# Performance work log

Hardware: AMD Instinct MI355X
Metric: run time of the kernel (lower is better)

Reference implementation:

```python
import jax, jax.numpy as jnp
import numpy as np

N = 50000      # nodes
E = 600000     # edges (before self-loops)
F_IN = 128     # num_node_features
HID = 64       # hidden_channels
HEADS = 4      # num_heads
ACT = 32       # action_dim
SENT = 768     # sentence embedding dim (fc1 input)


def setup_inputs() -> dict:
    key = jax.random.key(0)
    ks = jax.random.split(key, 32)
    rn = lambda k, s, sc=0.05: jax.random.normal(k, s, jnp.float32) * sc
    return {
        "x": jax.random.normal(ks[0], (N, F_IN), jnp.float32),
        "edge_index": jax.random.randint(ks[1], (2, E), 0, N, dtype=jnp.int32),
        "sentence_emb": jax.random.normal(ks[2], (1, SENT), jnp.float32),
        "active_node_idx": 123,
        "step": 3,
        # conv1: GATConv(F_IN -> HID, heads=HEADS, concat=True)
        "W1": rn(ks[3], (F_IN, HEADS * HID)),
        "att_src1": rn(ks[4], (HEADS, HID)),
        "att_dst1": rn(ks[5], (HEADS, HID)),
        "b1": jnp.zeros((HEADS * HID,), jnp.float32),
        # conv2: GATConv(HEADS*HID -> HID, heads=1, concat=False)
        "W2": rn(ks[6], (HEADS * HID, HID)),
        "att_src2": rn(ks[7], (1, HID)),
        "att_dst2": rn(ks[8], (1, HID)),
        "b2": jnp.zeros((HID,), jnp.float32),
        "fc0_w": rn(ks[9], (1, HID)), "fc0_b": jnp.zeros((HID,), jnp.float32),
        "fc1_w": rn(ks[10], (SENT, HID)), "fc1_b": jnp.zeros((HID,), jnp.float32),
        "fc2_w": rn(ks[11], (HID, HID)), "fc2_b": jnp.zeros((HID,), jnp.float32),
        "fc3_w": rn(ks[12], (2 * HID, HID)), "fc3_b": jnp.zeros((HID,), jnp.float32),
        "val_w": rn(ks[13], (HID, 1)), "val_b": jnp.zeros((1,), jnp.float32),
        "adv_w": rn(ks[14], (HID, ACT)), "adv_b": jnp.zeros((ACT,), jnp.float32),
        "ln_h_g": jnp.ones((HID,), jnp.float32), "ln_h_b": jnp.zeros((HID,), jnp.float32),
        "ln_f_g": jnp.ones((2 * HID,), jnp.float32), "ln_f_b": jnp.zeros((2 * HID,), jnp.float32),
        "ln_a_g": jnp.ones((HEADS * HID,), jnp.float32), "ln_a_b": jnp.zeros((HEADS * HID,), jnp.float32),
    }


def layernorm(x, g, b, eps=1e-5):
    mu = jnp.mean(x, axis=-1, keepdims=True)
    var = jnp.mean((x - mu) ** 2, axis=-1, keepdims=True)
    return (x - mu) / jnp.sqrt(var + eps) * g + b


def gat_layer(h_in, src, dst, W, a_src, a_dst, bias, concat):
    """PyG GATConv (eval mode): gather -> edge score -> segment softmax -> scatter-add."""
    n = h_in.shape[0]
    heads, ch = a_src.shape
    h = (h_in @ W).reshape(n, heads, ch)                      # [N,H,C]
    es = jnp.einsum('nhc,hc->nh', h, a_src)                   # alpha_src per node
    ed = jnp.einsum('nhc,hc->nh', h, a_dst)                   # alpha_dst per node
    e = jax.nn.leaky_relu(es[src] + ed[dst], 0.2)             # [Etot,H]
    m = jax.ops.segment_max(e, dst, num_segments=n)           # stable softmax per dst
    ex = jnp.exp(e - m[dst])
    denom = jax.ops.segment_sum(ex, dst, num_segments=n) + 1e-16
    alpha = ex / denom[dst]                                   # [Etot,H]
    out = jax.ops.segment_sum(h[src] * alpha[:, :, None], dst, num_segments=n)
    out = out.reshape(n, heads * ch) if concat else out.mean(axis=1)
    return out + bias, alpha


def reference(x, edge_index, sentence_emb, active_node_idx, step,
              W1, att_src1, att_dst1, b1, W2, att_src2, att_dst2, b2,
              fc0_w, fc0_b, fc1_w, fc1_b, fc2_w, fc2_b, fc3_w, fc3_b,
              val_w, val_b, adv_w, adv_b,
              ln_h_g, ln_h_b, ln_f_g, ln_f_b, ln_a_g, ln_a_b):
    n = x.shape[0]
    loops = jnp.arange(n, dtype=edge_index.dtype)             # PyG add_self_loops=True
    src = jnp.concatenate([edge_index[0], loops])
    dst = jnp.concatenate([edge_index[1], loops])

    # step embedding: fc0((step+1)*0.01) -> relu -> LN
    steps = jnp.full((1, 1), (step + 1) * 0.01, jnp.float32)
    steps = layernorm(jax.nn.relu(steps @ fc0_w + fc0_b), ln_h_g, ln_h_b)

    # sentence embedding path (F.normalize result is discarded in the original)
    sent = layernorm(jax.nn.relu(sentence_emb @ fc1_w + fc1_b), ln_h_g, ln_h_b)
    sent = sent + steps
    sent = layernorm(jax.nn.relu(sent @ fc2_w + fc2_b), ln_h_g, ln_h_b)

    # two GAT layers
    h1, _ = gat_layer(x, src, dst, W1, att_src1, att_dst1, b1, concat=True)
    h1 = layernorm(jax.nn.elu(h1), ln_a_g, ln_a_b)
    h2, alpha = gat_layer(h1, src, dst, W2, att_src2, att_dst2, b2, concat=False)
    h2 = layernorm(h2, ln_h_g, ln_h_b)

    # dueling head on active node
    anf = jnp.concatenate([h2[active_node_idx][None, :], sent], axis=1)   # [1, 2*HID]
    anf = layernorm(anf, ln_f_g, ln_f_b)
    anf = layernorm(jax.nn.relu(anf @ fc3_w + fc3_b), ln_h_g, ln_h_b)
    val = anf @ val_w + val_b
    adv = anf @ adv_w + adv_b
    logits = jnp.tanh(val + adv - adv.mean())
    return logits, h2, alpha
```

## Files before the change

kernel.cpp:

```cpp
#include <hip/hip_runtime.h>
#include <cstdint>
#include <cstddef>

#define DEV __device__ __forceinline__

static constexpr int NN  = 50000;
static constexpr int EE  = 600000;
static constexpr int ET  = 650000;
static constexpr int SCAN_CHUNK = 1024;
static constexpr int SCAN_NB = (NN + SCAN_CHUNK - 1) / SCAN_CHUNK;

typedef __attribute__((ext_vector_type(8))) short bf16x8;
typedef __attribute__((ext_vector_type(4))) float f32x4;
typedef __attribute__((ext_vector_type(4))) int   i32x4;

DEV float wsum(float v){
  #pragma unroll
  for (int o = 32; o > 0; o >>= 1) v += __shfl_xor(v, o, 64);
  return v;
}
DEV float wmaxr(float v){
  #pragma unroll
  for (int o = 32; o > 0; o >>= 1) v = fmaxf(v, __shfl_xor(v, o, 64));
  return v;
}
DEV float lrelu(float x){ return x > 0.f ? x : 0.2f * x; }
DEV float eluf(float x){ return x > 0.f ? x : expm1f(x); }
DEV float ln64(float v, const float* g, const float* b, int lane){
  float mu  = wsum(v) * (1.f/64.f);
  float d   = v - mu;
  float var = wsum(d*d) * (1.f/64.f);
  return d * rsqrtf(var + 1e-5f) * g[lane] + b[lane];
}
DEV unsigned int bf16u(float f){
  unsigned int u = __float_as_uint(f);
  return (u + 0x7fffu + ((u >> 16) & 1u)) >> 16;
}
DEV float bfl(unsigned int lo16){ return __uint_as_float(lo16 << 16); }

__global__ void degree_kernel(const int* __restrict__ ei, int* __restrict__ deg){
  int e = blockIdx.x * blockDim.x + threadIdx.x;
  if (e >= ET) return;
  int dst = (e < EE) ? ei[EE + e] : (e - EE);
  atomicAdd(&deg[dst], 1);
}

__global__ __launch_bounds__(256) void scan_part(const int* __restrict__ deg,
                                                 int* __restrict__ off,
                                                 int* __restrict__ bsum, int n){
  __shared__ int wtot[4];
  int tid = threadIdx.x, lane = tid & 63, w = tid >> 6;
  int i0 = blockIdx.x * SCAN_CHUNK + tid * 4;
  int v[4], s = 0;
  #pragma unroll
  for (int p = 0; p < 4; p++){ int i = i0 + p; v[p] = (i < n) ? deg[i] : 0; s += v[p]; }
  int sc = s;
  #pragma unroll
  for (int d = 1; d < 64; d <<= 1){ int t = __shfl_up(sc, d, 64); if (lane >= d) sc += t; }
  if (lane == 63) wtot[w] = sc;
  __syncthreads();
  int woff = 0;
  #pragma unroll
  for (int k = 0; k < 4; k++) if (k < w) woff += wtot[k];
  int excl = woff + sc - s;
  #pragma unroll
  for (int p = 0; p < 4; p++){
    int i = i0 + p;
    if (i < n) off[i] = excl;
    excl += v[p];
  }
  if (tid == 0) bsum[blockIdx.x] = wtot[0] + wtot[1] + wtot[2] + wtot[3];
}

__global__ __launch_bounds__(64) void scan_top(int* __restrict__ bsum, int nb){
  int lane = threadIdx.x;
  int v = (lane < nb) ? bsum[lane] : 0;
  int sc = v;
  #pragma unroll
  for (int d = 1; d < 64; d <<= 1){ int t = __shfl_up(sc, d, 64); if (lane >= d) sc += t; }
  if (lane < nb) bsum[lane] = sc - v;
  if (lane == 63) bsum[nb] = sc;
}

__global__ __launch_bounds__(256) void scan_add(int* __restrict__ off,
                                                int* __restrict__ cur,
                                                const int* __restrict__ bsum, int n, int nb){
  int i0 = blockIdx.x * SCAN_CHUNK + threadIdx.x * 4;
  int add = bsum[blockIdx.x];
  #pragma unroll
  for (int p = 0; p < 4; p++){
    int j = i0 + p;
    if (j < n){ int t = off[j] + add; off[j] = t; cur[j] = t; }
  }
  if (blockIdx.x == 0 && threadIdx.x == 0) off[n] = bsum[nb];
}

__global__ void fill_csr(const int* __restrict__ ei, int* __restrict__ cur,
                         int* __restrict__ csr_src, int* __restrict__ csr_eid){
  int e = blockIdx.x * blockDim.x + threadIdx.x;
  if (e >= ET) return;
  int src, dst;
  if (e < EE){ src = ei[e]; dst = ei[EE + e]; } else { src = dst = e - EE; }
  int pos = atomicAdd(&cur[dst], 1);
  csr_src[pos] = src;
  csr_eid[pos] = e;
}

__global__ __launch_bounds__(256) void pack_w(const float* __restrict__ W,
                                              short* __restrict__ Wp, int K, int N){
  int tid = blockIdx.x * blockDim.x + threadIdx.x;
  int ksteps = K >> 5;
  int total = (N >> 4) * ksteps * 64;
  if (tid >= total) return;
  int lane = tid & 63;
  int ks   = (tid >> 6) % ksteps;
  int mb   = (tid >> 6) / ksteps;
  int col  = mb * 16 + (lane & 15);
  int krow = ks * 32 + (lane >> 4) * 8;
  short v[8];
  #pragma unroll
  for (int j = 0; j < 8; j++) v[j] = (short)bf16u(W[(size_t)(krow + j) * N + col]);
  #pragma unroll
  for (int j = 0; j < 8; j++) Wp[(size_t)tid * 8 + j] = v[j];
}

template<int KSTEPS, int MBLKS, int NH, bool INF32>
__global__ __launch_bounds__(256) void mfma_gemm_att(const short* __restrict__ Wp,
                                                     const float* __restrict__ Xf,
                                                     const unsigned short* __restrict__ Xh,
                                                     unsigned short* __restrict__ Cb,
                                                     const float* __restrict__ asrc,
                                                     const float* __restrict__ adst,
                                                     float* __restrict__ es,
                                                     float* __restrict__ ed, int M){
  constexpr int K = KSTEPS * 32, N = MBLKS * 16;
  int lane  = threadIdx.x & 63;
  int wv    = threadIdx.x >> 6;
  int quad  = lane >> 4;
  int node  = blockIdx.x * 64 + wv * 16 + (lane & 15);
  bool nv   = node < M;
  int nodec = nv ? node : M - 1;

  f32x4 acc[MBLKS];
  #pragma unroll
  for (int m = 0; m < MBLKS; m++) acc[m] = (f32x4){0.f, 0.f, 0.f, 0.f};

  #pragma unroll
  for (int ks = 0; ks < KSTEPS; ks++){
    int k0 = ks * 32 + quad * 8;
    bf16x8 bfrag;
    if (INF32){
      float4 u = *(const float4*)(Xf + (size_t)nodec * K + k0);
      float4 v = *(const float4*)(Xf + (size_t)nodec * K + k0 + 4);
      i32x4 bi;
      bi.x = (int)(bf16u(u.x) | (bf16u(u.y) << 16));
      bi.y = (int)(bf16u(u.z) | (bf16u(u.w) << 16));
      bi.z = (int)(bf16u(v.x) | (bf16u(v.y) << 16));
      bi.w = (int)(bf16u(v.z) | (bf16u(v.w) << 16));
      bfrag = __builtin_bit_cast(bf16x8, bi);
    } else {
      bfrag = *(const bf16x8*)(Xh + (size_t)nodec * K + k0);
    }
    #pragma unroll
    for (int mb = 0; mb < MBLKS; mb++){
      bf16x8 afrag = *(const bf16x8*)(Wp + ((size_t)(mb * KSTEPS + ks) * 64 + lane) * 8);
      acc[mb] = __builtin_amdgcn_mfma_f32_16x16x32_bf16(afrag, bfrag, acc[mb], 0, 0, 0);
    }
  }

  if (nv){
    unsigned short* crow = Cb + (size_t)node * N;
    #pragma unroll
    for (int mb = 0; mb < MBLKS; mb++){
      uint2 p;
      p.x = bf16u(acc[mb][0]) | (bf16u(acc[mb][1]) << 16);
      p.y = bf16u(acc[mb][2]) | (bf16u(acc[mb][3]) << 16);
      *(uint2*)(crow + mb * 16 + quad * 4) = p;
    }
  }

  float ps[NH], pd[NH];
  #pragma unroll
  for (int h = 0; h < NH; h++){ ps[h] = 0.f; pd[h] = 0.f; }
  #pragma unroll
  for (int mb = 0; mb < MBLKS; mb++){
    int h = (NH == 1) ? 0 : (mb >> 2);
    #pragma unroll
    for (int r = 0; r < 4; r++){
      int c = mb * 16 + quad * 4 + r;
      ps[h] = fmaf(acc[mb][r], asrc[c], ps[h]);
      pd[h] = fmaf(acc[mb][r], adst[c], pd[h]);
    }
  }
  #pragma unroll
  for (int h = 0; h < NH; h++){
    ps[h] += __shfl_xor(ps[h], 16, 64); ps[h] += __shfl_xor(ps[h], 32, 64);
    pd[h] += __shfl_xor(pd[h], 16, 64); pd[h] += __shfl_xor(pd[h], 32, 64);
  }
  if (quad == 0 && nv){
    if (NH == 4){
      *(float4*)(es + (size_t)node * 4) = make_float4(ps[0], ps[1], ps[2], ps[3]);
      *(float4*)(ed + (size_t)node * 4) = make_float4(pd[0], pd[1], pd[2], pd[3]);
    } else {
      es[node] = ps[0];
      ed[node] = pd[0];
    }
  }
}

__global__ __launch_bounds__(256) void agg1_kernel(const int* __restrict__ off,
                                                   const int* __restrict__ csr_src,
                                                   const unsigned short* __restrict__ H1b,
                                                   const float* __restrict__ es,
                                                   const float* __restrict__ ed,
                                                   const float* __restrict__ b1,
                                                   const float* __restrict__ lng,
                                                   const float* __restrict__ lnb,
                                                   unsigned short* __restrict__ h1b, int n){
  __shared__ float wsh4[4][64][4];
  __shared__ int   ssh[4][64];
  int wv   = threadIdx.x >> 6;
  int wid  = (blockIdx.x * blockDim.x + threadIdx.x) >> 6;
  int lane = threadIdx.x & 63;
  if (wid >= n) return;
  int s0  = off[wid];
  int deg = off[wid + 1] - s0;
  const float4 edv = *(const float4*)(ed + (size_t)wid * 4);

  float v0, v1, v2, v3;

  if (deg <= 64){
    bool vld = lane < deg;
    int srcl = vld ? csr_src[s0 + lane] : 0;
    float4 e4 = vld ? *(const float4*)(es + (size_t)srcl * 4)
                    : make_float4(-1e30f, -1e30f, -1e30f, -1e30f);
    float e0 = vld ? lrelu(e4.x + edv.x) : -1e30f;
    float e1 = vld ? lrelu(e4.y + edv.y) : -1e30f;
    float e2 = vld ? lrelu(e4.z + edv.z) : -1e30f;
    float e3 = vld ? lrelu(e4.w + edv.w) : -1e30f;
    float m0 = wmaxr(e0), m1 = wmaxr(e1), m2 = wmaxr(e2), m3 = wmaxr(e3);
    float w0 = vld ? __expf(e0 - m0) : 0.f;
    float w1 = vld ? __expf(e1 - m1) : 0.f;
    float w2 = vld ? __expf(e2 - m2) : 0.f;
    float w3 = vld ? __expf(e3 - m3) : 0.f;
    w0 /= (wsum(w0) + 1e-16f);
    w1 /= (wsum(w1) + 1e-16f);
    w2 /= (wsum(w2) + 1e-16f);
    w3 /= (wsum(w3) + 1e-16f);
    ssh[wv][lane] = srcl;
    *(float4*)&wsh4[wv][lane][0] = make_float4(w0, w1, w2, w3);
    __builtin_amdgcn_wave_barrier();

    int h = lane >> 4;
    float ax = 0.f, ay = 0.f, az = 0.f, aw = 0.f;
    int t = 0;
    for (; t + 4 <= deg; t += 4){
      int a0 = ssh[wv][t],     a1 = ssh[wv][t + 1];
      int a2 = ssh[wv][t + 2], a3 = ssh[wv][t + 3];
      float q0 = wsh4[wv][t][h],     q1 = wsh4[wv][t + 1][h];
      float q2 = wsh4[wv][t + 2][h], q3 = wsh4[wv][t + 3][h];
      uint2 g0 = *(const uint2*)(H1b + (size_t)a0 * 256 + lane * 4);
      uint2 g1 = *(const uint2*)(H1b + (size_t)a1 * 256 + lane * 4);
      uint2 g2 = *(const uint2*)(H1b + (size_t)a2 * 256 + lane * 4);
      uint2 g3 = *(const uint2*)(H1b + (size_t)a3 * 256 + lane * 4);
      ax = fmaf(__uint_as_float(g0.x << 16),        q0, ax);
      ay = fmaf(__uint_as_float(g0.x & 0xffff0000u), q0, ay);
      az = fmaf(__uint_as_float(g0.y << 16),        q0, az);
      aw = fmaf(__uint_as_float(g0.y & 0xffff0000u), q0, aw);
      ax = fmaf(__uint_as_float(g1.x << 16),        q1, ax);
      ay = fmaf(__uint_as_float(g1.x & 0xffff0000u), q1, ay);
      az = fmaf(__uint_as_float(g1.y << 16),        q1, az);
      aw = fmaf(__uint_as_float(g1.y & 0xffff0000u), q1, aw);
      ax = fmaf(__uint_as_float(g2.x << 16),        q2, ax);
      ay = fmaf(__uint_as_float(g2.x & 0xffff0000u), q2, ay);
      az = fmaf(__uint_as_float(g2.y << 16),        q2, az);
      aw = fmaf(__uint_as_float(g2.y & 0xffff0000u), q2, aw);
      ax = fmaf(__uint_as_float(g3.x << 16),        q3, ax);
      ay = fmaf(__uint_as_float(g3.x & 0xffff0000u), q3, ay);
      az = fmaf(__uint_as_float(g3.y << 16),        q3, az);
      aw = fmaf(__uint_as_float(g3.y & 0xffff0000u), q3, aw);
    }
    for (; t < deg; t++){
      int a0 = ssh[wv][t];
      float q0 = wsh4[wv][t][h];
      uint2 g0 = *(const uint2*)(H1b + (size_t)a0 * 256 + lane * 4);
      ax = fmaf(__uint_as_float(g0.x << 16),        q0, ax);
      ay = fmaf(__uint_as_float(g0.x & 0xffff0000u), q0, ay);
      az = fmaf(__uint_as_float(g0.y << 16),        q0, az);
      aw = fmaf(__uint_as_float(g0.y & 0xffff0000u), q0, aw);
    }
    float4 bb = *(const float4*)(b1 + lane * 4);
    v0 = eluf(ax + bb.x); v1 = eluf(ay + bb.y);
    v2 = eluf(az + bb.z); v3 = eluf(aw + bb.w);
    float mu = wsum(v0 + v1 + v2 + v3) * (1.f/256.f);
    float q  = (v0-mu)*(v0-mu) + (v1-mu)*(v1-mu) + (v2-mu)*(v2-mu) + (v3-mu)*(v3-mu);
    float rstd = rsqrtf(wsum(q) * (1.f/256.f) + 1e-5f);
    float4 g4 = *(const float4*)(lng + lane * 4);
    float4 bo = *(const float4*)(lnb + lane * 4);
    uint2 p;
    p.x = bf16u((v0-mu)*rstd*g4.x + bo.x) | (bf16u((v1-mu)*rstd*g4.y + bo.y) << 16);
    p.y = bf16u((v2-mu)*rstd*g4.z + bo.z) | (bf16u((v3-mu)*rstd*g4.w + bo.w) << 16);
    *(uint2*)(h1b + (size_t)wid * 256 + lane * 4) = p;
    return;
  }

  float m0 = -1e30f, m1 = -1e30f, m2 = -1e30f, m3 = -1e30f;
  for (int j = lane; j < deg; j += 64){
    int src = csr_src[s0 + j];
    float4 e4 = *(const float4*)(es + (size_t)src * 4);
    m0 = fmaxf(m0, lrelu(e4.x + edv.x));
    m1 = fmaxf(m1, lrelu(e4.y + edv.y));
    m2 = fmaxf(m2, lrelu(e4.z + edv.z));
    m3 = fmaxf(m3, lrelu(e4.w + edv.w));
  }
  m0 = wmaxr(m0); m1 = wmaxr(m1); m2 = wmaxr(m2); m3 = wmaxr(m3);
  float acc0 = 0.f, acc1 = 0.f, acc2 = 0.f, acc3 = 0.f;
  float den0 = 0.f, den1 = 0.f, den2 = 0.f, den3 = 0.f;
  for (int j = 0; j < deg; j++){
    int src = csr_src[s0 + j];
    float4 e4 = *(const float4*)(es + (size_t)src * 4);
    float x0 = __expf(lrelu(e4.x + edv.x) - m0);
    float x1 = __expf(lrelu(e4.y + edv.y) - m1);
    float x2 = __expf(lrelu(e4.z + edv.z) - m2);
    float x3 = __expf(lrelu(e4.w + edv.w) - m3);
    den0 += x0; den1 += x1; den2 += x2; den3 += x3;
    const unsigned short* hp = H1b + (size_t)src * 256;
    acc0 = fmaf(bfl(hp[lane]),       x0, acc0);
    acc1 = fmaf(bfl(hp[64 + lane]),  x1, acc1);
    acc2 = fmaf(bfl(hp[128 + lane]), x2, acc2);
    acc3 = fmaf(bfl(hp[192 + lane]), x3, acc3);
  }
  v0 = eluf(acc0 / (den0 + 1e-16f) + b1[lane]);
  v1 = eluf(acc1 / (den1 + 1e-16f) + b1[64 + lane]);
  v2 = eluf(acc2 / (den2 + 1e-16f) + b1[128 + lane]);
  v3 = eluf(acc3 / (den3 + 1e-16f) + b1[192 + lane]);
  float mu = wsum(v0 + v1 + v2 + v3) * (1.f/256.f);
  float q  = (v0-mu)*(v0-mu) + (v1-mu)*(v1-mu) + (v2-mu)*(v2-mu) + (v3-mu)*(v3-mu);
  float rstd = rsqrtf(wsum(q) * (1.f/256.f) + 1e-5f);
  unsigned short* o = h1b + (size_t)wid * 256;
  o[lane]       = (unsigned short)bf16u((v0-mu)*rstd*lng[lane]       + lnb[lane]);
  o[64 + lane]  = (unsigned short)bf16u((v1-mu)*rstd*lng[64 + lane]  + lnb[64 + lane]);
  o[128 + lane] = (unsigned short)bf16u((v2-mu)*rstd*lng[128 + lane] + lnb[128 + lane]);
  o[192 + lane] = (unsigned short)bf16u((v3-mu)*rstd*lng[192 + lane] + lnb[192 + lane]);
}

__global__ __launch_bounds__(256) void agg2_kernel(const int* __restrict__ off,
                                                   const int* __restrict__ csr_src,
                                                   const int* __restrict__ csr_eid,
                                                   const unsigned short* __restrict__ H2b,
                                                   const float* __restrict__ es,
                                                   const float* __restrict__ ed,
                                                   const float* __restrict__ b2,
                                                   const float* __restrict__ lng,
                                                   const float* __restrict__ lnb,
                                                   float* __restrict__ h2out,
                                                   float* __restrict__ alpha_out, int n){
  int wid  = (blockIdx.x * blockDim.x + threadIdx.x) >> 6;
  int lane = threadIdx.x & 63;
  if (wid >= n) return;
  int s0  = off[wid];
  int deg = off[wid + 1] - s0;
  float edv = ed[wid];
  float acc = 0.f;

  if (deg <= 64){
    bool vld = lane < deg;
    int srcl = vld ? csr_src[s0 + lane] : 0;
    float el = vld ? lrelu(es[srcl] + edv) : -1e30f;
    float m  = wmaxr(el);
    float w  = vld ? __expf(el - m) : 0.f;
    float den = wsum(w) + 1e-16f;
    float wl = w / den;
    if (vld) alpha_out[csr_eid[s0 + lane]] = wl;
    int t = 0;
    for (; t + 4 <= deg; t += 4){
      int a0 = __shfl(srcl, t, 64),   a1 = __shfl(srcl, t+1, 64);
      int a2 = __shfl(srcl, t+2, 64), a3 = __shfl(srcl, t+3, 64);
      float q0 = __shfl(wl, t, 64),   q1 = __shfl(wl, t+1, 64);
      float q2 = __shfl(wl, t+2, 64), q3 = __shfl(wl, t+3, 64);
      float h0 = bfl(H2b[(size_t)a0 * 64 + lane]);
      float h1v = bfl(H2b[(size_t)a1 * 64 + lane]);
      float h2v = bfl(H2b[(size_t)a2 * 64 + lane]);
      float h3 = bfl(H2b[(size_t)a3 * 64 + lane]);
      acc = fmaf(h0, q0, acc); acc = fmaf(h1v, q1, acc);
      acc = fmaf(h2v, q2, acc); acc = fmaf(h3, q3, acc);
    }
    for (; t < deg; t++){
      int a0 = __shfl(srcl, t, 64);
      float q0 = __shfl(wl, t, 64);
      acc = fmaf(bfl(H2b[(size_t)a0 * 64 + lane]), q0, acc);
    }
  } else {
    float m = -1e30f;
    for (int j = lane; j < deg; j += 64){
      int src = csr_src[s0 + j];
      m = fmaxf(m, lrelu(es[src] + edv));
    }
    m = wmaxr(m);
    float den = 0.f;
    for (int j = lane; j < deg; j += 64){
      int src = csr_src[s0 + j];
      den += __expf(lrelu(es[src] + edv) - m);
    }
    den = wsum(den) + 1e-16f;
    for (int j = 0; j < deg; j++){
      int src = csr_src[s0 + j];
      float a = __expf(lrelu(es[src] + edv) - m) / den;
      if (lane == 0) alpha_out[csr_eid[s0 + j]] = a;
      acc = fmaf(bfl(H2b[(size_t)src * 64 + lane]), a, acc);
    }
  }
  float v  = acc + b2[lane];
  float mu = wsum(v) * (1.f/64.f);
  float d  = v - mu;
  float rstd = rsqrtf(wsum(d*d) * (1.f/64.f) + 1e-5f);
  h2out[(size_t)wid * 64 + lane] = d * rstd * lng[lane] + lnb[lane];
}

__global__ __launch_bounds__(64) void head_kernel(const float* __restrict__ semb,
                                                  const int* __restrict__ active,
                                                  const int* __restrict__ step,
                                                  const float* __restrict__ fc0w, const float* __restrict__ fc0b,
                                                  const float* __restrict__ fc1w, const float* __restrict__ fc1b,
                                                  const float* __restrict__ fc2w, const float* __restrict__ fc2b,
                                                  const float* __restrict__ fc3w, const float* __restrict__ fc3b,
                                                  const float* __restrict__ valw, const float* __restrict__ valb,
                                                  const float* __restrict__ advw, const float* __restrict__ advb,
                                                  const float* __restrict__ lnhg, const float* __restrict__ lnhb,
                                                  const float* __restrict__ lnfg, const float* __restrict__ lnfb,
                                                  const float* __restrict__ h2,
                                                  float* __restrict__ out){
  int t = threadIdx.x;
  __shared__ float sh[128];

  float sval = (float)(step[0] + 1) * 0.01f;
  float stepsv = ln64(fmaxf(fmaf(sval, fc0w[t], fc0b[t]), 0.f), lnhg, lnhb, t);

  float acc = fc1b[t];
  #pragma unroll 8
  for (int k = 0; k < 768; k++) acc = fmaf(semb[k], fc1w[k * 64 + t], acc);
  float sentv = ln64(fmaxf(acc, 0.f), lnhg, lnhb, t) + stepsv;
  sh[t] = sentv;
  __syncthreads();
  float acc2 = fc2b[t];
  #pragma unroll 8
  for (int k = 0; k < 64; k++) acc2 = fmaf(sh[k], fc2w[k * 64 + t], acc2);
  __syncthreads();
  float sent2 = ln64(fmaxf(acc2, 0.f), lnhg, lnhb, t);

  float a0 = h2[(size_t)active[0] * 64 + t];
  float a1 = sent2;
  float mu = wsum(a0 + a1) * (1.f/128.f);
  float q  = (a0-mu)*(a0-mu) + (a1-mu)*(a1-mu);
  float rstd = rsqrtf(wsum(q) * (1.f/128.f) + 1e-5f);
  float n0 = (a0-mu)*rstd*lnfg[t]      + lnfb[t];
  float n1 = (a1-mu)*rstd*lnfg[64 + t] + lnfb[64 + t];
  sh[t] = n0; sh[64 + t] = n1;
  __syncthreads();

  float acc3 = fc3b[t];
  #pragma unroll 8
  for (int k = 0; k < 128; k++) acc3 = fmaf(sh[k], fc3w[k * 64 + t], acc3);
  float a2v = ln64(fmaxf(acc3, 0.f), lnhg, lnhb, t);
  __syncthreads();
  sh[t] = a2v;
  __syncthreads();

  float val = wsum(a2v * valw[t]) + valb[0];
  float advv = 0.f;
  if (t < 32){
    advv = advb[t];
    #pragma unroll 8
    for (int k = 0; k < 64; k++) advv = fmaf(sh[k], advw[k * 32 + t], advv);
  }
  float am = wsum(t < 32 ? advv : 0.f) * (1.f/32.f);
  if (t < 32) out[t] = tanhf(val + advv - am);
}

extern "C" void kernel_launch(void* const* d_in, const int* in_sizes, int n_in,
                              void* d_out, int out_size, void* d_ws, size_t ws_size,
                              hipStream_t stream) {
  const float* x     = (const float*)d_in[0];
  const int*   ei    = (const int*)  d_in[1];
  const float* semb  = (const float*)d_in[2];
  const int*   act   = (const int*)  d_in[3];
  const int*   step  = (const int*)  d_in[4];
  const float* W1    = (const float*)d_in[5];
  const float* as1   = (const float*)d_in[6];
  const float* ad1   = (const float*)d_in[7];
  const float* b1    = (const float*)d_in[8];
  const float* W2    = (const float*)d_in[9];
  const float* as2   = (const float*)d_in[10];
  const float* ad2   = (const float*)d_in[11];
  const float* b2    = (const float*)d_in[12];
  const float* fc0w  = (const float*)d_in[13];
  const float* fc0b  = (const float*)d_in[14];
  const float* fc1w  = (const float*)d_in[15];
  const float* fc1b  = (const float*)d_in[16];
  const float* fc2w  = (const float*)d_in[17];
  const float* fc2b  = (const float*)d_in[18];
  const float* fc3w  = (const float*)d_in[19];
  const float* fc3b  = (const float*)d_in[20];
  const float* valw  = (const float*)d_in[21];
  const float* valb  = (const float*)d_in[22];
  const float* advw  = (const float*)d_in[23];
  const float* advb  = (const float*)d_in[24];
  const float* lnhg  = (const float*)d_in[25];
  const float* lnhb  = (const float*)d_in[26];
  const float* lnfg  = (const float*)d_in[27];
  const float* lnfb  = (const float*)d_in[28];
  const float* lnag  = (const float*)d_in[29];
  const float* lnab  = (const float*)d_in[30];

  char* ws = (char*)d_ws;
  size_t o = 0;
  auto alloc = [&](size_t bytes) -> void* {
    o = (o + 255) & ~(size_t)255;
    void* p = ws + o;
    o += bytes;
    return p;
  };
  int*   deg     = (int*)  alloc((size_t)(NN + 1) * 4);
  int*   off     = (int*)  alloc((size_t)(NN + 1) * 4);
  int*   cur     = (int*)  alloc((size_t)NN * 4);
  int*   bsum    = (int*)  alloc((size_t)(SCAN_NB + 1) * 4);
  int*   csr_src = (int*)  alloc((size_t)ET * 4);
  int*   csr_eid = (int*)  alloc((size_t)ET * 4);
  short* Wp1     = (short*)alloc((size_t)16 * 4 * 64 * 8 * 2);
  short* Wp2     = (short*)alloc((size_t)4 * 8 * 64 * 8 * 2);
  unsigned short* H1b = (unsigned short*)alloc((size_t)NN * 256 * 2);
  unsigned short* h1b = (unsigned short*)alloc((size_t)NN * 256 * 2);
  float* es1     = (float*)alloc((size_t)NN * 16);
  float* ed1     = (float*)alloc((size_t)NN * 16);
  unsigned short* H2b = H1b;
  float* es2 = es1;
  float* ed2 = ed1;

  float* logits    = (float*)d_out;
  float* h2out     = (float*)d_out + 32;
  float* alpha_out = (float*)d_out + 32 + (size_t)NN * 64;

  hipMemsetAsync(deg, 0, (size_t)NN * 4, stream);
  degree_kernel<<<(ET + 255) / 256, 256, 0, stream>>>(ei, deg);
  scan_part<<<SCAN_NB, 256, 0, stream>>>(deg, off, bsum, NN);
  scan_top <<<1, 64, 0, stream>>>(bsum, SCAN_NB);
  scan_add <<<SCAN_NB, 256, 0, stream>>>(off, cur, bsum, NN, SCAN_NB);
  fill_csr<<<(ET + 255) / 256, 256, 0, stream>>>(ei, cur, csr_src, csr_eid);

  pack_w<<<16, 256, 0, stream>>>(W1, Wp1, 128, 256);
  pack_w<<<8, 256, 0, stream>>>(W2, Wp2, 256, 64);

  mfma_gemm_att<4, 16, 4, true><<<(NN + 63) / 64, 256, 0, stream>>>(
      Wp1, x, nullptr, H1b, as1, ad1, es1, ed1, NN);
  agg1_kernel<<<NN / 4, 256, 0, stream>>>(off, csr_src, H1b, es1, ed1, b1, lnag, lnab, h1b, NN);

  mfma_gemm_att<8, 4, 1, false><<<(NN + 63) / 64, 256, 0, stream>>>(
      Wp2, nullptr, h1b, H2b, as2, ad2, es2, ed2, NN);
  agg2_kernel<<<NN / 4, 256, 0, stream>>>(off, csr_src, csr_eid, H2b, es2, ed2, b2,
                                          lnhg, lnhb, h2out, alpha_out, NN);

  head_kernel<<<1, 64, 0, stream>>>(semb, act, step,
                                    fc0w, fc0b, fc1w, fc1b, fc2w, fc2b, fc3w, fc3b,
                                    valw, valb, advw, advb,
                                    lnhg, lnhb, lnfg, lnfb,
                                    h2out, logits);
}
```

Before: 393.5 us.

## Fuse CSR build into cooperative kernel, fuse head into agg2, retune aggregation loops

Replaces the memset, degree, three scan kernels, CSR fill and two weight-pack kernels with a single cooperative kernel that uses grid-wide syncs between phases, cutting launch overhead. The dueling head is folded into the second aggregation kernel and runs on the wave that owns the active node. The first aggregation now stores attention weights transposed and unrolls the gather by 8 with vector LDS loads. The second aggregation has each wave handle feature pairs per half-wave. In exchange, grid.sync costs and a 256-block cooperative grid limit parallelism for the atomic phases, and the head adds serial work inside one wave of agg2.

```diff
diff --git a/kernel.cpp b/kernel.cpp
--- a/kernel.cpp
+++ b/kernel.cpp
@@ -1,6 +1,9 @@
 #include <hip/hip_runtime.h>
+#include <hip/hip_cooperative_groups.h>
 #include <cstdint>
 #include <cstddef>
+
+namespace cg = cooperative_groups;
 
 #define DEV __device__ __forceinline__
 
@@ -38,90 +41,101 @@
 }
 DEV float bfl(unsigned int lo16){ return __uint_as_float(lo16 << 16); }
 
-__global__ void degree_kernel(const int* __restrict__ ei, int* __restrict__ deg){
-  int e = blockIdx.x * blockDim.x + threadIdx.x;
-  if (e >= ET) return;
-  int dst = (e < EE) ? ei[EE + e] : (e - EE);
-  atomicAdd(&deg[dst], 1);
-}
-
-__global__ __launch_bounds__(256) void scan_part(const int* __restrict__ deg,
-                                                 int* __restrict__ off,
-                                                 int* __restrict__ bsum, int n){
+__global__ __launch_bounds__(256) void prep_kernel(const int* __restrict__ ei,
+                                                   const float* __restrict__ W1,
+                                                   const float* __restrict__ W2,
+                                                   int* __restrict__ deg,
+                                                   int* __restrict__ off,
+                                                   int* __restrict__ cur,
+                                                   int* __restrict__ bsum,
+                                                   int* __restrict__ csr_src,
+                                                   int* __restrict__ csr_eid,
+                                                   short* __restrict__ Wp1,
+                                                   short* __restrict__ Wp2){
+  cg::grid_group grid = cg::this_grid();
+  const int tid = blockIdx.x * 256 + threadIdx.x;
   __shared__ int wtot[4];
-  int tid = threadIdx.x, lane = tid & 63, w = tid >> 6;
-  int i0 = blockIdx.x * SCAN_CHUNK + tid * 4;
-  int v[4], s = 0;
-  #pragma unroll
-  for (int p = 0; p < 4; p++){ int i = i0 + p; v[p] = (i < n) ? deg[i] : 0; s += v[p]; }
-  int sc = s;
-  #pragma unroll
-  for (int d = 1; d < 64; d <<= 1){ int t = __shfl_up(sc, d, 64); if (lane >= d) sc += t; }
-  if (lane == 63) wtot[w] = sc;
-  __syncthreads();
-  int woff = 0;
-  #pragma unroll
-  for (int k = 0; k < 4; k++) if (k < w) woff += wtot[k];
-  int excl = woff + sc - s;
-  #pragma unroll
-  for (int p = 0; p < 4; p++){
-    int i = i0 + p;
-    if (i < n) off[i] = excl;
-    excl += v[p];
-  }
-  if (tid == 0) bsum[blockIdx.x] = wtot[0] + wtot[1] + wtot[2] + wtot[3];
-}
-
-__global__ __launch_bounds__(64) void scan_top(int* __restrict__ bsum, int nb){
-  int lane = threadIdx.x;
-  int v = (lane < nb) ? bsum[lane] : 0;
-  int sc = v;
-  #pragma unroll
-  for (int d = 1; d < 64; d <<= 1){ int t = __shfl_up(sc, d, 64); if (lane >= d) sc += t; }
-  if (lane < nb) bsum[lane] = sc - v;
-  if (lane == 63) bsum[nb] = sc;
-}
-
-__global__ __launch_bounds__(256) void scan_add(int* __restrict__ off,
-                                                int* __restrict__ cur,
-                                                const int* __restrict__ bsum, int n, int nb){
-  int i0 = blockIdx.x * SCAN_CHUNK + threadIdx.x * 4;
-  int add = bsum[blockIdx.x];
-  #pragma unroll
-  for (int p = 0; p < 4; p++){
-    int j = i0 + p;
-    if (j < n){ int t = off[j] + add; off[j] = t; cur[j] = t; }
-  }
-  if (blockIdx.x == 0 && threadIdx.x == 0) off[n] = bsum[nb];
-}
-
-__global__ void fill_csr(const int* __restrict__ ei, int* __restrict__ cur,
-                         int* __restrict__ csr_src, int* __restrict__ csr_eid){
-  int e = blockIdx.x * blockDim.x + threadIdx.x;
-  if (e >= ET) return;
-  int src, dst;
-  if (e < EE){ src = ei[e]; dst = ei[EE + e]; } else { src = dst = e - EE; }
-  int pos = atomicAdd(&cur[dst], 1);
-  csr_src[pos] = src;
-  csr_eid[pos] = e;
-}
-
-__global__ __launch_bounds__(256) void pack_w(const float* __restrict__ W,
-                                              short* __restrict__ Wp, int K, int N){
-  int tid = blockIdx.x * blockDim.x + threadIdx.x;
-  int ksteps = K >> 5;
-  int total = (N >> 4) * ksteps * 64;
-  if (tid >= total) return;
-  int lane = tid & 63;
-  int ks   = (tid >> 6) % ksteps;
-  int mb   = (tid >> 6) / ksteps;
-  int col  = mb * 16 + (lane & 15);
-  int krow = ks * 32 + (lane >> 4) * 8;
-  short v[8];
-  #pragma unroll
-  for (int j = 0; j < 8; j++) v[j] = (short)bf16u(W[(size_t)(krow + j) * N + col]);
-  #pragma unroll
-  for (int j = 0; j < 8; j++) Wp[(size_t)tid * 8 + j] = v[j];
+
+  for (int i = tid; i <= NN; i += 65536) deg[i] = 0;
+  if (tid < 4096){
+    int lane = tid & 63, ks = (tid >> 6) & 3, mb = tid >> 8;
+    int col  = mb * 16 + (lane & 15);
+    int krow = ks * 32 + (lane >> 4) * 8;
+    #pragma unroll
+    for (int j = 0; j < 8; j++)
+      Wp1[(size_t)tid * 8 + j] = (short)bf16u(W1[(size_t)(krow + j) * 256 + col]);
+  } else if (tid < 4096 + 2048){
+    int t2 = tid - 4096;
+    int lane = t2 & 63, ks = (t2 >> 6) & 7, mb = t2 >> 9;
+    int col  = mb * 16 + (lane & 15);
+    int krow = ks * 32 + (lane >> 4) * 8;
+    #pragma unroll
+    for (int j = 0; j < 8; j++)
+      Wp2[(size_t)t2 * 8 + j] = (short)bf16u(W2[(size_t)(krow + j) * 64 + col]);
+  }
+  grid.sync();
+
+  for (int e = tid; e < ET; e += 65536){
+    int dst = (e < EE) ? ei[EE + e] : (e - EE);
+    atomicAdd(&deg[dst], 1);
+  }
+  grid.sync();
+
+  if (blockIdx.x < SCAN_NB){
+    int t = threadIdx.x, lane = t & 63, w = t >> 6;
+    int i0 = blockIdx.x * SCAN_CHUNK + t * 4;
+    int v[4], s = 0;
+    #pragma unroll
+    for (int p = 0; p < 4; p++){ int i = i0 + p; v[p] = (i < NN) ? deg[i] : 0; s += v[p]; }
+    int sc = s;
+    #pragma unroll
+    for (int d = 1; d < 64; d <<= 1){ int u = __shfl_up(sc, d, 64); if (lane >= d) sc += u; }
+    if (lane == 63) wtot[w] = sc;
+    __syncthreads();
+    int woff = 0;
+    #pragma unroll
+    for (int k = 0; k < 4; k++) if (k < w) woff += wtot[k];
+    int excl = woff + sc - s;
+    #pragma unroll
+    for (int p = 0; p < 4; p++){
+      int i = i0 + p;
+      if (i < NN) off[i] = excl;
+      excl += v[p];
+    }
+    if (t == 0) bsum[blockIdx.x] = wtot[0] + wtot[1] + wtot[2] + wtot[3];
+  }
+  grid.sync();
+
+  if (blockIdx.x == 0 && threadIdx.x < 64){
+    int lane = threadIdx.x;
+    int v = (lane < SCAN_NB) ? bsum[lane] : 0;
+    int sc = v;
+    #pragma unroll
+    for (int d = 1; d < 64; d <<= 1){ int u = __shfl_up(sc, d, 64); if (lane >= d) sc += u; }
+    if (lane < SCAN_NB) bsum[lane] = sc - v;
+    if (lane == 63) bsum[SCAN_NB] = sc;
+  }
+  grid.sync();
+
+  if (blockIdx.x < SCAN_NB){
+    int i0 = blockIdx.x * SCAN_CHUNK + threadIdx.x * 4;
+    int add = bsum[blockIdx.x];
+    #pragma unroll
+    for (int p = 0; p < 4; p++){
+      int j = i0 + p;
+      if (j < NN){ int u = off[j] + add; off[j] = u; cur[j] = u; }
+    }
+    if (blockIdx.x == 0 && threadIdx.x == 0) off[NN] = bsum[SCAN_NB];
+  }
+  grid.sync();
+
+  for (int e = tid; e < ET; e += 65536){
+    int src, dst;
+    if (e < EE){ src = ei[e]; dst = ei[EE + e]; } else { src = dst = e - EE; }
+    int pos = atomicAdd(&cur[dst], 1);
+    csr_src[pos] = src;
+    csr_eid[pos] = e;
+  }
 }
 
 template<int KSTEPS, int MBLKS, int NH, bool INF32>
@@ -208,6 +222,13 @@
   }
 }
 
+DEV void acc4u(uint2 g, float q, float& ax, float& ay, float& az, float& aw){
+  ax = fmaf(__uint_as_float(g.x << 16),         q, ax);
+  ay = fmaf(__uint_as_float(g.x & 0xffff0000u), q, ay);
+  az = fmaf(__uint_as_float(g.y << 16),         q, az);
+  aw = fmaf(__uint_as_float(g.y & 0xffff0000u), q, aw);
+}
+
 __global__ __launch_bounds__(256) void agg1_kernel(const int* __restrict__ off,
                                                    const int* __restrict__ csr_src,
                                                    const unsigned short* __restrict__ H1b,
@@ -217,7 +238,7 @@
                                                    const float* __restrict__ lng,
                                                    const float* __restrict__ lnb,
                                                    unsigned short* __restrict__ h1b, int n){
-  __shared__ float wsh4[4][64][4];
+  __shared__ float wshT[4][4][68];
   __shared__ int   ssh[4][64];
   int wv   = threadIdx.x >> 6;
   int wid  = (blockIdx.x * blockDim.x + threadIdx.x) >> 6;
@@ -248,59 +269,55 @@
     w2 /= (wsum(w2) + 1e-16f);
     w3 /= (wsum(w3) + 1e-16f);
     ssh[wv][lane] = srcl;
-    *(float4*)&wsh4[wv][lane][0] = make_float4(w0, w1, w2, w3);
+    wshT[wv][0][lane] = w0; wshT[wv][1][lane] = w1;
+    wshT[wv][2][lane] = w2; wshT[wv][3][lane] = w3;
     __builtin_amdgcn_wave_barrier();
 
     int h = lane >> 4;
+    const float* wrow = &wshT[wv][h][0];
+    int lane4 = lane * 4;
     float ax = 0.f, ay = 0.f, az = 0.f, aw = 0.f;
     int t = 0;
-    for (; t + 4 <= deg; t += 4){
-      int a0 = ssh[wv][t],     a1 = ssh[wv][t + 1];
-      int a2 = ssh[wv][t + 2], a3 = ssh[wv][t + 3];
-      float q0 = wsh4[wv][t][h],     q1 = wsh4[wv][t + 1][h];
-      float q2 = wsh4[wv][t + 2][h], q3 = wsh4[wv][t + 3][h];
-      uint2 g0 = *(const uint2*)(H1b + (size_t)a0 * 256 + lane * 4);
-      uint2 g1 = *(const uint2*)(H1b + (size_t)a1 * 256 + lane * 4);
-      uint2 g2 = *(const uint2*)(H1b + (size_t)a2 * 256 + lane * 4);
-      uint2 g3 = *(const uint2*)(H1b + (size_t)a3 * 256 + lane * 4);
-      ax = fmaf(__uint_as_float(g0.x << 16),        q0, ax);
-      ay = fmaf(__uint_as_float(g0.x & 0xffff0000u), q0, ay);
-      az = fmaf(__uint_as_float(g0.y << 16),        q0, az);
-      aw = fmaf(__uint_as_float(g0.y & 0xffff0000u), q0, aw);
-      ax = fmaf(__uint_as_float(g1.x << 16),        q1, ax);
-      ay = fmaf(__uint_as_float(g1.x & 0xffff0000u), q1, ay);
-      az = fmaf(__uint_as_float(g1.y << 16),        q1, az);
-      aw = fmaf(__uint_as_float(g1.y & 0xffff0000u), q1, aw);
-      ax = fmaf(__uint_as_float(g2.x << 16),        q2, ax);
-      ay = fmaf(__uint_as_float(g2.x & 0xffff0000u), q2, ay);
-      az = fmaf(__uint_as_float(g2.y << 16),        q2, az);
-      aw = fmaf(__uint_as_float(g2.y & 0xffff0000u), q2, aw);
-      ax = fmaf(__uint_as_float(g3.x << 16),        q3, ax);
-      ay = fmaf(__uint_as_float(g3.x & 0xffff0000u), q3, ay);
-      az = fmaf(__uint_as_float(g3.y << 16),        q3, az);
-      aw = fmaf(__uint_as_float(g3.y & 0xffff0000u), q3, aw);
+    for (; t + 8 <= deg; t += 8){
+      i32x4 sA = *(const i32x4*)&ssh[wv][t];
+      i32x4 sB = *(const i32x4*)&ssh[wv][t + 4];
+      f32x4 qA = *(const f32x4*)&wrow[t];
+      f32x4 qB = *(const f32x4*)&wrow[t + 4];
+      uint2 g0 = *(const uint2*)(H1b + (size_t)sA.x * 256 + lane4);
+      uint2 g1 = *(const uint2*)(H1b + (size_t)sA.y * 256 + lane4);
+      uint2 g2 = *(const uint2*)(H1b + (size_t)sA.z * 256 + lane4);
+      uint2 g3 = *(const uint2*)(H1b + (size_t)sA.w * 256 + lane4);
+      uint2 g4 = *(const uint2*)(H1b + (size_t)sB.x * 256 + lane4);
+      uint2 g5 = *(const uint2*)(H1b + (size_t)sB.y * 256 + lane4);
+      uint2 g6 = *(const uint2*)(H1b + (size_t)sB.z * 256 + lane4);
+      uint2 g7 = *(const uint2*)(H1b + (size_t)sB.w * 256 + lane4);
+      acc4u(g0, qA.x, ax, ay, az, aw);
+      acc4u(g1, qA.y, ax, ay, az, aw);
+      acc4u(g2, qA.z, ax, ay, az, aw);
+      acc4u(g3, qA.w, ax, ay, az, aw);
+      acc4u(g4, qB.x, ax, ay, az, aw);
+      acc4u(g5, qB.y, ax, ay, az, aw);
+      acc4u(g6, qB.z, ax, ay, az, aw);
+      acc4u(g7, qB.w, ax, ay, az, aw);
     }
     for (; t < deg; t++){
       int a0 = ssh[wv][t];
-      float q0 = wsh4[wv][t][h];
-      uint2 g0 = *(const uint2*)(H1b + (size_t)a0 * 256 + lane * 4);
-      ax = fmaf(__uint_as_float(g0.x << 16),        q0, ax);
-      ay = fmaf(__uint_as_float(g0.x & 0xffff0000u), q0, ay);
-      az = fmaf(__uint_as_float(g0.y << 16),        q0, az);
-      aw = fmaf(__uint_as_float(g0.y & 0xffff0000u), q0, aw);
-    }
-    float4 bb = *(const float4*)(b1 + lane * 4);
+      float q0 = wrow[t];
+      uint2 g0 = *(const uint2*)(H1b + (size_t)a0 * 256 + lane4);
+      acc4u(g0, q0, ax, ay, az, aw);
+    }
+    float4 bb = *(const float4*)(b1 + lane4);
     v0 = eluf(ax + bb.x); v1 = eluf(ay + bb.y);
     v2 = eluf(az + bb.z); v3 = eluf(aw + bb.w);
     float mu = wsum(v0 + v1 + v2 + v3) * (1.f/256.f);
     float q  = (v0-mu)*(v0-mu) + (v1-mu)*(v1-mu) + (v2-mu)*(v2-mu) + (v3-mu)*(v3-mu);
     float rstd = rsqrtf(wsum(q) * (1.f/256.f) + 1e-5f);
-    float4 g4 = *(const float4*)(lng + lane * 4);
-    float4 bo = *(const float4*)(lnb + lane * 4);
+    float4 g4v = *(const float4*)(lng + lane4);
+    float4 bo  = *(const float4*)(lnb + lane4);
     uint2 p;
-    p.x = bf16u((v0-mu)*rstd*g4.x + bo.x) | (bf16u((v1-mu)*rstd*g4.y + bo.y) << 16);
-    p.y = bf16u((v2-mu)*rstd*g4.z + bo.z) | (bf16u((v3-mu)*rstd*g4.w + bo.w) << 16);
-    *(uint2*)(h1b + (size_t)wid * 256 + lane * 4) = p;
+    p.x = bf16u((v0-mu)*rstd*g4v.x + bo.x) | (bf16u((v1-mu)*rstd*g4v.y + bo.y) << 16);
+    p.y = bf16u((v2-mu)*rstd*g4v.z + bo.z) | (bf16u((v3-mu)*rstd*g4v.w + bo.w) << 16);
+    *(uint2*)(h1b + (size_t)wid * 256 + lane4) = p;
     return;
   }
 
@@ -344,24 +361,42 @@
   o[192 + lane] = (unsigned short)bf16u((v3-mu)*rstd*lng[192 + lane] + lnb[192 + lane]);
 }
 
-__global__ __launch_bounds__(256) void agg2_kernel(const int* __restrict__ off,
-                                                   const int* __restrict__ csr_src,
-                                                   const int* __restrict__ csr_eid,
-                                                   const unsigned short* __restrict__ H2b,
-                                                   const float* __restrict__ es,
-                                                   const float* __restrict__ ed,
-                                                   const float* __restrict__ b2,
-                                                   const float* __restrict__ lng,
-                                                   const float* __restrict__ lnb,
-                                                   float* __restrict__ h2out,
-                                                   float* __restrict__ alpha_out, int n){
+__global__ __launch_bounds__(256) void agg2_head(const int* __restrict__ off,
+                                                 const int* __restrict__ csr_src,
+                                                 const int* __restrict__ csr_eid,
+                                                 const unsigned short* __restrict__ H2b,
+                                                 const float* __restrict__ es,
+                                                 const float* __restrict__ ed,
+                                                 const float* __restrict__ b2,
+                                                 const float* __restrict__ lng,
+                                                 const float* __restrict__ lnb,
+                                                 const float* __restrict__ semb,
+                                                 const int* __restrict__ active,
+                                                 const int* __restrict__ stepp,
+                                                 const float* __restrict__ fc0w, const float* __restrict__ fc0b,
+                                                 const float* __restrict__ fc1w, const float* __restrict__ fc1b,
+                                                 const float* __restrict__ fc2w, const float* __restrict__ fc2b,
+                                                 const float* __restrict__ fc3w, const float* __restrict__ fc3b,
+                                                 const float* __restrict__ valw, const float* __restrict__ valb,
+                                                 const float* __restrict__ advw, const float* __restrict__ advb,
+                                                 const float* __restrict__ lnhg, const float* __restrict__ lnhb,
+                                                 const float* __restrict__ lnfg, const float* __restrict__ lnfb,
+                                                 float* __restrict__ h2out,
+                                                 float* __restrict__ alpha_out,
+                                                 float* __restrict__ logits, int n){
+  __shared__ float wsa[4][64];
+  __shared__ int   ssa[4][64];
+  __shared__ float shh[192];
+  int wv   = threadIdx.x >> 6;
   int wid  = (blockIdx.x * blockDim.x + threadIdx.x) >> 6;
   int lane = threadIdx.x & 63;
   if (wid >= n) return;
   int s0  = off[wid];
   int deg = off[wid + 1] - s0;
   float edv = ed[wid];
-  float acc = 0.f;
+  int sub = lane & 31, half = lane >> 5;
+  const unsigned short* base = H2b + sub * 2;
+  float va, vb;
 
   if (deg <= 64){
     bool vld = lane < deg;
@@ -372,109 +407,120 @@
     float den = wsum(w) + 1e-16f;
     float wl = w / den;
     if (vld) alpha_out[csr_eid[s0 + lane]] = wl;
-    int t = 0;
-    for (; t + 4 <= deg; t += 4){
-      int a0 = __shfl(srcl, t, 64),   a1 = __shfl(srcl, t+1, 64);
-      int a2 = __shfl(srcl, t+2, 64), a3 = __shfl(srcl, t+3, 64);
-      float q0 = __shfl(wl, t, 64),   q1 = __shfl(wl, t+1, 64);
-      float q2 = __shfl(wl, t+2, 64), q3 = __shfl(wl, t+3, 64);
-      float h0 = bfl(H2b[(size_t)a0 * 64 + lane]);
-      float h1v = bfl(H2b[(size_t)a1 * 64 + lane]);
-      float h2v = bfl(H2b[(size_t)a2 * 64 + lane]);
-      float h3 = bfl(H2b[(size_t)a3 * 64 + lane]);
-      acc = fmaf(h0, q0, acc); acc = fmaf(h1v, q1, acc);
-      acc = fmaf(h2v, q2, acc); acc = fmaf(h3, q3, acc);
-    }
-    for (; t < deg; t++){
-      int a0 = __shfl(srcl, t, 64);
-      float q0 = __shfl(wl, t, 64);
-      acc = fmaf(bfl(H2b[(size_t)a0 * 64 + lane]), q0, acc);
-    }
+    ssa[wv][lane] = srcl;
+    wsa[wv][lane] = vld ? wl : 0.f;
+    __builtin_amdgcn_wave_barrier();
+
+    float a0 = 0.f, a1 = 0.f;
+    int nsteps = (deg + 1) >> 1;
+    int j = 0;
+    for (; j + 4 <= nsteps; j += 4){
+      int e0 = 2 * j + half;
+      int sA = ssa[wv][e0],     sB = ssa[wv][e0 + 2];
+      int sC = ssa[wv][e0 + 4], sD = ssa[wv][e0 + 6];
+      float wA = wsa[wv][e0],     wB = wsa[wv][e0 + 2];
+      float wC = wsa[wv][e0 + 4], wD = wsa[wv][e0 + 6];
+      unsigned int gA = *(const unsigned int*)(base + (size_t)sA * 64);
+      unsigned int gB = *(const unsigned int*)(base + (size_t)sB * 64);
+      unsigned int gC = *(const unsigned int*)(base + (size_t)sC * 64);
+      unsigned int gD = *(const unsigned int*)(base + (size_t)sD * 64);
+      a0 = fmaf(__uint_as_float(gA << 16),         wA, a0);
+      a1 = fmaf(__uint_as_float(gA & 0xffff0000u), wA, a1);
+      a0 = fmaf(__uint_as_float(gB << 16),         wB, a0);
+      a1 = fmaf(__uint_as_float(gB & 0xffff0000u), wB, a1);
+      a0 = fmaf(__uint_as_float(gC << 16),         wC, a0);
+      a1 = fmaf(__uint_as_float(gC & 0xffff0000u), wC, a1);
+      a0 = fmaf(__uint_as_float(gD << 16),         wD, a0);
+      a1 = fmaf(__uint_as_float(gD & 0xffff0000u), wD, a1);
+    }
+    for (; j < nsteps; j++){
+      int e = 2 * j + half;
+      int sA = ssa[wv][e];
+      float wA = wsa[wv][e];
+      unsigned int g = *(const unsigned int*)(base + (size_t)sA * 64);
+      a0 = fmaf(__uint_as_float(g << 16),         wA, a0);
+      a1 = fmaf(__uint_as_float(g & 0xffff0000u), wA, a1);
+    }
+    a0 += __shfl_xor(a0, 32, 64);
+    a1 += __shfl_xor(a1, 32, 64);
+    va = a0 + b2[2 * sub];
+    vb = a1 + b2[2 * sub + 1];
   } else {
     float m = -1e30f;
-    for (int j = lane; j < deg; j += 64){
-      int src = csr_src[s0 + j];
-      m = fmaxf(m, lrelu(es[src] + edv));
-    }
+    for (int j2 = lane; j2 < deg; j2 += 64)
+      m = fmaxf(m, lrelu(es[csr_src[s0 + j2]] + edv));
     m = wmaxr(m);
     float den = 0.f;
-    for (int j = lane; j < deg; j += 64){
-      int src = csr_src[s0 + j];
-      den += __expf(lrelu(es[src] + edv) - m);
-    }
+    for (int j2 = lane; j2 < deg; j2 += 64)
+      den += __expf(lrelu(es[csr_src[s0 + j2]] + edv) - m);
     den = wsum(den) + 1e-16f;
-    for (int j = 0; j < deg; j++){
-      int src = csr_src[s0 + j];
-      float a = __expf(lrelu(es[src] + edv) - m) / den;
-      if (lane == 0) alpha_out[csr_eid[s0 + j]] = a;
-      acc = fmaf(bfl(H2b[(size_t)src * 64 + lane]), a, acc);
-    }
-  }
-  float v  = acc + b2[lane];
-  float mu = wsum(v) * (1.f/64.f);
-  float d  = v - mu;
-  float rstd = rsqrtf(wsum(d*d) * (1.f/64.f) + 1e-5f);
-  h2out[(size_t)wid * 64 + lane] = d * rstd * lng[lane] + lnb[lane];
-}
-
-__global__ __launch_bounds__(64) void head_kernel(const float* __restrict__ semb,
-                                                  const int* __restrict__ active,
-                                                  const int* __restrict__ step,
-                                                  const float* __restrict__ fc0w, const float* __restrict__ fc0b,
-                                                  const float* __restrict__ fc1w, const float* __restrict__ fc1b,
-                                                  const float* __restrict__ fc2w, const float* __restrict__ fc2b,
-                                                  const float* __restrict__ fc3w, const float* __restrict__ fc3b,
-                                                  const float* __restrict__ valw, const float* __restrict__ valb,
-                                                  const float* __restrict__ advw, const float* __restrict__ advb,
-                                                  const float* __restrict__ lnhg, const float* __restrict__ lnhb,
-                                                  const float* __restrict__ lnfg, const float* __restrict__ lnfb,
-                                                  const float* __restrict__ h2,
-                                                  float* __restrict__ out){
-  int t = threadIdx.x;
-  __shared__ float sh[128];
-
-  float sval = (float)(step[0] + 1) * 0.01f;
-  float stepsv = ln64(fmaxf(fmaf(sval, fc0w[t], fc0b[t]), 0.f), lnhg, lnhb, t);
-
-  float acc = fc1b[t];
-  #pragma unroll 8
-  for (int k = 0; k < 768; k++) acc = fmaf(semb[k], fc1w[k * 64 + t], acc);
-  float sentv = ln64(fmaxf(acc, 0.f), lnhg, lnhb, t) + stepsv;
-  sh[t] = sentv;
-  __syncthreads();
-  float acc2 = fc2b[t];
-  #pragma unroll 8
-  for (int k = 0; k < 64; k++) acc2 = fmaf(sh[k], fc2w[k * 64 + t], acc2);
-  __syncthreads();
-  float sent2 = ln64(fmaxf(acc2, 0.f), lnhg, lnhb, t);
-
-  float a0 = h2[(size_t)active[0] * 64 + t];
-  float a1 = sent2;
-  float mu = wsum(a0 + a1) * (1.f/128.f);
-  float q  = (a0-mu)*(a0-mu) + (a1-mu)*(a1-mu);
-  float rstd = rsqrtf(wsum(q) * (1.f/128.f) + 1e-5f);
-  float n0 = (a0-mu)*rstd*lnfg[t]      + lnfb[t];
-  float n1 = (a1-mu)*rstd*lnfg[64 + t] + lnfb[64 + t];
-  sh[t] = n0; sh[64 + t] = n1;
-  __syncthreads();
-
-  float acc3 = fc3b[t];
-  #pragma unroll 8
-  for (int k = 0; k < 128; k++) acc3 = fmaf(sh[k], fc3w[k * 64 + t], acc3);
-  float a2v = ln64(fmaxf(acc3, 0.f), lnhg, lnhb, t);
-  __syncthreads();
-  sh[t] = a2v;
-  __syncthreads();
-
-  float val = wsum(a2v * valw[t]) + valb[0];
-  float advv = 0.f;
-  if (t < 32){
-    advv = advb[t];
+    float a0 = 0.f, a1 = 0.f;
+    for (int j2 = 0; j2 < deg; j2++){
+      int srcj = csr_src[s0 + j2];
+      float a = __expf(lrelu(es[srcj] + edv) - m) / den;
+      if (lane == 0) alpha_out[csr_eid[s0 + j2]] = a;
+      unsigned int g = *(const unsigned int*)(base + (size_t)srcj * 64);
+      a0 = fmaf(__uint_as_float(g << 16),         a, a0);
+      a1 = fmaf(__uint_as_float(g & 0xffff0000u), a, a1);
+    }
+    va = a0 + b2[2 * sub];
+    vb = a1 + b2[2 * sub + 1];
+  }
+
+  float mu = wsum(va + vb) * (1.f/128.f);
+  float d0 = va - mu, d1 = vb - mu;
+  float rstd = rsqrtf(wsum(d0*d0 + d1*d1) * (1.f/128.f) + 1e-5f);
+  float n0v = d0 * rstd * lng[2 * sub]     + lnb[2 * sub];
+  float n1v = d1 * rstd * lng[2 * sub + 1] + lnb[2 * sub + 1];
+  if (half == 0)
+    *(float2*)(h2out + (size_t)wid * 64 + 2 * sub) = make_float2(n0v, n1v);
+
+  if (wid == active[0]){
+    int t = lane;
+    float ra = __shfl(n0v, t >> 1, 64);
+    float rb = __shfl(n1v, t >> 1, 64);
+    float h2t = (t & 1) ? rb : ra;
+
+    float sval = (float)(stepp[0] + 1) * 0.01f;
+    float stepsv = ln64(fmaxf(fmaf(sval, fc0w[t], fc0b[t]), 0.f), lnhg, lnhb, t);
+
+    float acc = fc1b[t];
     #pragma unroll 8
-    for (int k = 0; k < 64; k++) advv = fmaf(sh[k], advw[k * 32 + t], advv);
-  }
-  float am = wsum(t < 32 ? advv : 0.f) * (1.f/32.f);
-  if (t < 32) out[t] = tanhf(val + advv - am);
+    for (int k = 0; k < 768; k++) acc = fmaf(semb[k], fc1w[k * 64 + t], acc);
+    float sentv = ln64(fmaxf(acc, 0.f), lnhg, lnhb, t) + stepsv;
+    shh[t] = sentv;
+    __builtin_amdgcn_wave_barrier();
+    float acc2 = fc2b[t];
+    #pragma unroll 8
+    for (int k = 0; k < 64; k++) acc2 = fmaf(shh[k], fc2w[k * 64 + t], acc2);
+    __builtin_amdgcn_wave_barrier();
+    float sent2 = ln64(fmaxf(acc2, 0.f), lnhg, lnhb, t);
+
+    float c0 = h2t, c1 = sent2;
+    float mu2 = wsum(c0 + c1) * (1.f/128.f);
+    float q2  = (c0-mu2)*(c0-mu2) + (c1-mu2)*(c1-mu2);
+    float rs2 = rsqrtf(wsum(q2) * (1.f/128.f) + 1e-5f);
+    shh[t]      = (c0-mu2)*rs2*lnfg[t]      + lnfb[t];
+    shh[64 + t] = (c1-mu2)*rs2*lnfg[64 + t] + lnfb[64 + t];
+    __builtin_amdgcn_wave_barrier();
+
+    float acc3 = fc3b[t];
+    #pragma unroll 8
+    for (int k = 0; k < 128; k++) acc3 = fmaf(shh[k], fc3w[k * 64 + t], acc3);
+    float a2v = ln64(fmaxf(acc3, 0.f), lnhg, lnhb, t);
+    shh[128 + t] = a2v;
+    __builtin_amdgcn_wave_barrier();
+
+    float val = wsum(a2v * valw[t]) + valb[0];
+    float advv = 0.f;
+    if (t < 32){
+      advv = advb[t];
+      #pragma unroll 8
+      for (int k = 0; k < 64; k++) advv = fmaf(shh[128 + k], advw[k * 32 + t], advv);
+    }
+    float am = wsum(t < 32 ? advv : 0.f) * (1.f/32.f);
+    if (t < 32) logits[t] = tanhf(val + advv - am);
+  }
 }
 
 extern "C" void kernel_launch(void* const* d_in, const int* in_sizes, int n_in,
@@ -526,8 +572,8 @@
   int*   bsum    = (int*)  alloc((size_t)(SCAN_NB + 1) * 4);
   int*   csr_src = (int*)  alloc((size_t)ET * 4);
   int*   csr_eid = (int*)  alloc((size_t)ET * 4);
-  short* Wp1     = (short*)alloc((size_t)16 * 4 * 64 * 8 * 2);
-  short* Wp2     = (short*)alloc((size_t)4 * 8 * 64 * 8 * 2);
+  short* Wp1     = (short*)alloc((size_t)4096 * 8 * 2);
+  short* Wp2     = (short*)alloc((size_t)2048 * 8 * 2);
   unsigned short* H1b = (unsigned short*)alloc((size_t)NN * 256 * 2);
   unsigned short* h1b = (unsigned short*)alloc((size_t)NN * 256 * 2);
   float* es1     = (float*)alloc((size_t)NN * 16);
@@ -540,15 +586,12 @@
   float* h2out     = (float*)d_out + 32;
   float* alpha_out = (float*)d_out + 32 + (size_t)NN * 64;
 
-  hipMemsetAsync(deg, 0, (size_t)NN * 4, stream);
-  degree_kernel<<<(ET + 255) / 256, 256, 0, stream>>>(ei, deg);
-  scan_part<<<SCAN_NB, 256, 0, stream>>>(deg, off, bsum, NN);
-  scan_top <<<1, 64, 0, stream>>>(bsum, SCAN_NB);
-  scan_add <<<SCAN_NB, 256, 0, stream>>>(off, cur, bsum, NN, SCAN_NB);
-  fill_csr<<<(ET + 255) / 256, 256, 0, stream>>>(ei, cur, csr_src, csr_eid);
-
-  pack_w<<<16, 256, 0, stream>>>(W1, Wp1, 128, 256);
-  pack_w<<<8, 256, 0, stream>>>(W2, Wp2, 256, 64);
+  {
+    void* args[] = { (void*)&ei, (void*)&W1, (void*)&W2,
+                     (void*)&deg, (void*)&off, (void*)&cur, (void*)&bsum,
+                     (void*)&csr_src, (void*)&csr_eid, (void*)&Wp1, (void*)&Wp2 };
+    hipLaunchCooperativeKernel((void*)prep_kernel, dim3(256), dim3(256), args, 0, stream);
+  }
 
   mfma_gemm_att<4, 16, 4, true><<<(NN + 63) / 64, 256, 0, stream>>>(
       Wp1, x, nullptr, H1b, as1, ad1, es1, ed1, NN);
@@ -556,12 +599,11 @@
 
   mfma_gemm_att<8, 4, 1, false><<<(NN + 63) / 64, 256, 0, stream>>>(
       Wp2, nullptr, h1b, H2b, as2, ad2, es2, ed2, NN);
-  agg2_kernel<<<NN / 4, 256, 0, stream>>>(off, csr_src, csr_eid, H2b, es2, ed2, b2,
-                                          lnhg, lnhb, h2out, alpha_out, NN);
-
-  head_kernel<<<1, 64, 0, stream>>>(semb, act, step,
-                                    fc0w, fc0b, fc1w, fc1b, fc2w, fc2b, fc3w, fc3b,
-                                    valw, valb, advw, advb,
-                                    lnhg, lnhb, lnfg, lnfb,
-                                    h2out, logits);
-}
+  agg2_head<<<NN / 4, 256, 0, stream>>>(off, csr_src, csr_eid, H2b, es2, ed2, b2,
+                                        lnhg, lnhb,
+                                        semb, act, step,
+                                        fc0w, fc0b, fc1w, fc1b, fc2w, fc2b, fc3w, fc3b,
+                                        valw, valb, advw, advb,
+                                        lnhg, lnhb, lnfg, lnfb,
+                                        h2out, alpha_out, logits, NN);
+}
```

After: 551.7 us. 1.4x slower.
